# Kernel tuning notes

Measured on AMD Instinct MI355X. Metric: run time of the kernel, lower is better.

The kernel has to match this reference:

```python
import jax, jax.numpy as jnp
import numpy as np

# Module constants (from init_kwargs / defaults)
OUT_SIZE = (4, 32, 32)      # (Z, X, Y) grid
REAL_SIZE = (3.0, 25.0, 25.0)
SCALE = 1.4
THRESHOLD = 0.5
D_ELEMS = np.array([0.74 * SCALE, 0.528 * SCALE], dtype=np.float32)  # per-element match/NMS radius (O, H)


def _transform(x):
    """(B, X, Y, Z, 4*E) -> coords (B, E, N, 3), conf (B, E, N); N = Z*X*Y."""
    B, X, Y, Z, L = x.shape
    E = L // 4
    v = x.reshape(B, X, Y, Z, E, 4).transpose(0, 4, 3, 1, 2, 5)   # (B,E,Z,X,Y,4)
    v = v[..., jnp.array([2, 0, 1, 3])]                            # reorder last dim
    Zs, Xs, Ys = OUT_SIZE
    ind = jnp.stack(jnp.meshgrid(jnp.arange(Zs), jnp.arange(Xs), jnp.arange(Ys), indexing='ij'),
                    axis=-1).astype(x.dtype)                       # (Z,X,Y,3) == torch nonzero of ones
    expand = jnp.array([r / o for o, r in zip(OUT_SIZE, REAL_SIZE)], dtype=x.dtype)
    coords = (v[..., :3] + ind) * expand
    conf = v[..., 3]
    N = Zs * Xs * Ys
    return coords.reshape(B, E, N, 3), conf.reshape(B, E, N)


def _sort_by_conf(coords, conf):
    order = jnp.argsort(-conf, axis=-1)
    coords = jnp.take_along_axis(coords, order[..., None], axis=2)
    conf = jnp.take_along_axis(conf, order, axis=-1)
    return coords, conf


def _nms(pts, valid, d):
    """Greedy sequential NMS on one (N,3) point set. Point b is suppressed if any
    still-selected earlier point a<b lies within distance d. Invalid points never suppress."""
    N = pts.shape[0]
    d2 = jnp.sum((pts[:, None, :] - pts[None, :, :]) ** 2, axis=-1)   # (N,N)
    ar = jnp.arange(N)
    M = (d2 < d * d) & valid[:, None] & valid[None, :] & (ar[:, None] < ar[None, :])

    def body(b, sel):
        return sel.at[b].set(~jnp.any(sel & M[:, b]))

    sel = jax.lax.fori_loop(0, N, body, jnp.ones((N,), bool))
    return sel & valid


def _match(P, T, keepP, keepT, d):
    """Greedy row-major bipartite matching: each pred (in order) grabs the first
    still-unmatched target within distance d. Returns (TP, FP, FN) masks."""
    N = P.shape[0]
    d2 = jnp.sum((P[:, None, :] - T[None, :, :]) ** 2, axis=-1)      # (N,N)
    D = (d2 < d * d) & keepP[:, None] & keepT[None, :]

    def body(a, carry):
        selP, selT = carry
        avail = D[a] & ~selT
        has = jnp.any(avail)
        j = jnp.argmax(avail)                    # first available target index
        selT = selT.at[j].set(selT[j] | has)
        selP = selP.at[a].set(has)
        return (selP, selT)

    selP, selT = jax.lax.fori_loop(0, N, body,
                                   (jnp.zeros((N,), bool), jnp.zeros((N,), bool)))
    return selP, keepP & ~selP, keepT & ~selT    # TP, FP, FN masks


def setup_inputs() -> dict:
    key = jax.random.key(0)
    k1, k2 = jax.random.split(key)
    B = 4
    predictions = jax.random.normal(k1, (B, 32, 32, 4, 8), dtype=jnp.float32)
    targets = jax.random.normal(k2, (B, 32, 32, 4, 8), dtype=jnp.float32)
    return {"predictions": predictions, "targets": targets}


def reference(predictions, targets):
    Pc, Pconf = _sort_by_conf(*_transform(predictions))   # (B,E,N,3), (B,E,N)
    Tc, Tconf = _sort_by_conf(*_transform(targets))
    validP = Pconf > THRESHOLD
    validT = Tconf > THRESHOLD
    d = jnp.asarray(D_ELEMS)                               # (E,)

    nms_be = jax.vmap(jax.vmap(_nms, in_axes=(0, 0, 0)), in_axes=(0, 0, None))
    keepP = nms_be(Pc, validP, d)                          # (B,E,N) bool
    keepT = nms_be(Tc, validT, d)

    match_be = jax.vmap(jax.vmap(_match, in_axes=(0, 0, 0, 0, 0)), in_axes=(0, 0, 0, 0, None))
    tp, fp, fn = match_be(Pc, Tc, keepP, keepT, d)         # (B,E,N) bool each

    # sorted real-space points, NMS-kept masks, and TP/FP/FN masks (fixed-shape
    # equivalents of the torch module's filtered P/T/TP/FP/FN lists)
    return Pc, Tc, keepP, keepT, tp, fp, fn
```

## Files before the change

kernel.cpp:

```cpp
#include <hip/hip_runtime.h>
#include <hip/hip_bf16.h>

#pragma clang fp contract(off)

#define NPTS 4096
#define BE   8
#define COORD_SZ (BE * NPTS * 3)
#define MASK_SZ  (BE * NPTS)
#define OFF_PC   0
#define OFF_TC   (COORD_SZ)
#define OFF_KP   (2 * COORD_SZ)
#define OFF_KT   (2 * COORD_SZ + MASK_SZ)
#define OFF_TP   (2 * COORD_SZ + 2 * MASK_SZ)
#define OFF_FP   (2 * COORD_SZ + 3 * MASK_SZ)
#define OFF_FN   (2 * COORD_SZ + 4 * MASK_SZ)

#define VCAP 1664
#define NW   26

#define WS_KEYS_OFF  0ull
#define WS_V_OFF     524288ull
#define WS_KEEP_OFF  524352ull
#define WS_PP_OFF    528448ull
#define WS_PT_OFF    6066240ull
#define WS_NEED      8835136ull

typedef unsigned long long u64;

__device__ __forceinline__ float get_dd(int e) {
    const float d0 = (float)(0.74 * 1.4);
    const float d1 = (float)(0.528 * 1.4);
    float d = (e == 0) ? d0 : d1;
    return d * d;
}

__global__ __launch_bounds__(1024)
void sort_kernel(const float* __restrict__ pred,
                 const float* __restrict__ targ,
                 float* __restrict__ out,
                 int* __restrict__ Vcnt) {
    __shared__ u64 bufA[NPTS], bufB[NPTS];
    __shared__ unsigned int hist[1024];
    __shared__ unsigned int offarr[1024];
    __shared__ int wsum[16];
    __shared__ int vtot;
    const int s = blockIdx.x;
    const int arr = s & 1, be = s >> 1;
    const int b = be >> 1, e = be & 1;
    const float* __restrict__ src = arr ? targ : pred;
    const int t = threadIdx.x;
    const int lane = t & 63, wv = t >> 6;

    if (t == 0) vtot = 0;
    for (int n = t; n < NPTS; n += 1024) {
        int z = n >> 10, r = n & 1023, x = r >> 5, y = r & 31;
        int base = (((b * 32 + x) * 32 + y) * 4 + z) * 8 + e * 4;
        float conf = src[base + 3];
        unsigned int bits = __float_as_uint(conf);
        unsigned int u = (bits & 0x80000000u) ? ~bits : (bits | 0x80000000u);
        bufA[n] = ((u64)(~u) << 32) | (unsigned int)n;
    }
    __syncthreads();

    const u64 lmask = (1ull << lane) - 1ull;
    for (int k = 0; k < 8; ++k) {
        u64* cur = (k & 1) ? bufB : bufA;
        u64* nxt = (k & 1) ? bufA : bufB;
        const int shift = 32 + (k << 2);
        hist[t] = 0u;
        __syncthreads();

        u64 item[4]; int dg[4]; int rnk[4];
        #pragma unroll
        for (int m = 0; m < 4; ++m) {
            u64 it = cur[m * 1024 + t];
            int d = (int)((it >> shift) & 15);
            u64 eq = ~0ull;
            #pragma unroll
            for (int bb = 0; bb < 4; ++bb) {
                u64 bal = __ballot((d >> bb) & 1);
                eq &= ((d >> bb) & 1) ? bal : ~bal;
            }
            int r = (int)__popcll(eq & lmask);
            if (r == 0) hist[d * 64 + m * 16 + wv] = (unsigned int)__popcll(eq);
            item[m] = it; dg[m] = d; rnk[m] = r;
        }
        __syncthreads();

        {
            int v = (int)hist[t];
            int inc = v;
            #pragma unroll
            for (int dd = 1; dd < 64; dd <<= 1) {
                int x2 = __shfl_up(inc, dd);
                if (lane >= dd) inc += x2;
            }
            if (lane == 63) wsum[wv] = inc;
            __syncthreads();
            if (t < 16) {
                int wtot = wsum[t]; int iv = wtot;
                #pragma unroll
                for (int dd = 1; dd < 16; dd <<= 1) {
                    int x2 = __shfl_up(iv, dd);
                    if (t >= dd) iv += x2;
                }
                wsum[t] = iv - wtot;
            }
            __syncthreads();
            offarr[t] = (unsigned int)(wsum[wv] + (inc - v));
        }
        __syncthreads();

        #pragma unroll
        for (int m = 0; m < 4; ++m) {
            int pos = (int)offarr[dg[m] * 64 + m * 16 + wv] + rnk[m];
            nxt[pos] = item[m];
        }
        __syncthreads();
    }

    int myv = 0;
    for (int p = t; p < NPTS; p += 1024) {
        u64 key = bufA[p];
        int n = (int)(key & 0xFFFFFFFFull);
        myv += ((unsigned int)(key >> 32) < 0x40FFFFFFu) ? 1 : 0;
        int z = n >> 10, rr = n & 1023, x = rr >> 5, y = rr & 31;
        int base = (((b * 32 + x) * 32 + y) * 4 + z) * 8 + e * 4;
        float r0 = src[base + 0], r1 = src[base + 1], r2 = src[base + 2];
        float c0 = (r2 + (float)z) * 0.75f;
        float c1 = (r0 + (float)x) * 0.78125f;
        float c2 = (r1 + (float)y) * 0.78125f;
        float* dst = out + (size_t)arr * COORD_SZ + ((size_t)be * NPTS + p) * 3;
        dst[0] = c0; dst[1] = c1; dst[2] = c2;
    }
    atomicAdd(&vtot, myv);
    __syncthreads();
    if (t == 0) Vcnt[s] = vtot;
}

__global__ __launch_bounds__(256)
void matrix_kernel(const float* __restrict__ out,
                   const int* __restrict__ Vcnt,
                   u64* __restrict__ ws64) {
    __shared__ float4 tcol[VCAP];
    __shared__ float rowc[64][3];
    const int bx = blockIdx.x;
    const int j = bx / 26, c = bx % 26;
    const int t = threadIdx.x;

    int sRow, sCol, e;
    u64* dstBase;
    if (j < 16) {
        sRow = j; sCol = j; e = (j >> 1) & 1;
        dstBase = ws64 + (WS_PP_OFF / 8) + (size_t)j * VCAP * NW;
    } else {
        int be = j - 16;
        sRow = be * 2 + 0; sCol = be * 2 + 1; e = be & 1;
        dstBase = ws64 + (WS_PT_OFF / 8) + (size_t)be * VCAP * NW;
    }
    int Vr = Vcnt[sRow]; if (Vr > VCAP) Vr = VCAP;
    int Vc = Vcnt[sCol]; if (Vc > VCAP) Vc = VCAP;
    const int rb = c * 64;
    if (rb >= Vr) return;
    const float dd = get_dd(e);

    const float* __restrict__ colc = out + (size_t)(sCol & 1) * COORD_SZ + (size_t)(sCol >> 1) * NPTS * 3;
    const float* __restrict__ rowp = out + (size_t)(sRow & 1) * COORD_SZ + (size_t)(sRow >> 1) * NPTS * 3;

    for (int idx = t; idx < Vc * 3; idx += 256) {
        float v = colc[idx];
        int p = idx / 3, k = idx % 3;
        ((float*)&tcol[p])[k] = v;
    }
    for (int idx = t; idx < 192; idx += 256) {
        int i = idx / 3, k = idx % 3;
        if (rb + i < Vr) rowc[i][k] = rowp[(rb + i) * 3 + k];
    }
    __syncthreads();

    const int NWc = (Vc + 63) >> 6;
    const int wlimit = (j < 16) ? (c + 1) : NWc;
    const int i = t & 63;
    const bool rowOK = (rb + i) < Vr;
    if (rowOK) {
        float ax = rowc[i][0], ay = rowc[i][1], az = rowc[i][2];
        u64* dstRow = dstBase + (size_t)(rb + i) * NW;
        for (int w = t >> 6; w < wlimit; w += 4) {
            int jbase = w << 6;
            int jmax = Vc - jbase; if (jmax > 64) jmax = 64;
            u64 m = 0ull;
            for (int jj = 0; jj < jmax; ++jj) {
                float4 tc = tcol[jbase + jj];
                float dx = ax - tc.x, dy = ay - tc.y, dz = az - tc.z;
                float d2 = dx * dx + dy * dy + dz * dz;
                m |= (d2 < dd) ? (1ull << jj) : 0ull;
            }
            dstRow[w] = m;
        }
    }
}

__global__ __launch_bounds__(1024)
void nms_rounds_kernel(float* __restrict__ out,
                       const int* __restrict__ Vcnt,
                       u64* __restrict__ ws64) {
    __shared__ u64 U[NW];
    __shared__ u64 K[NW];
    __shared__ int remaining;
    const int s = blockIdx.x;
    const int arr = s & 1, be = s >> 1;
    const int t = threadIdx.x;
    int V = Vcnt[s]; if (V > VCAP) V = VCAP;
    const u64* __restrict__ Mx = ws64 + (WS_PP_OFF / 8) + (size_t)s * VCAP * NW;

    if (t < NW) {
        int base = t << 6;
        int rem = V - base;
        u64 u = (rem >= 64) ? ~0ull : ((rem > 0) ? ((1ull << rem) - 1ull) : 0ull);
        U[t] = u;
        K[t] = 0ull;
    }
    if (t == 0) remaining = V;
    __syncthreads();

    while (remaining > 0) {
        bool dec0 = false, keep0 = false;
        bool dec1 = false, keep1 = false;

        {
            const int i = t;
            if (i < V && ((U[i >> 6] >> (i & 63)) & 1ull)) {
                const u64* __restrict__ row = Mx + (size_t)i * NW;
                const int wi = i >> 6;
                u64 cu = 0ull, ck = 0ull;
                int w = 0;
                for (; w + 4 <= wi; w += 4) {
                    u64 m0 = row[w], m1 = row[w + 1], m2 = row[w + 2], m3 = row[w + 3];
                    cu |= (m0 & U[w]) | (m1 & U[w + 1]) | (m2 & U[w + 2]) | (m3 & U[w + 3]);
                    ck |= (m0 & K[w]) | (m1 & K[w + 1]) | (m2 & K[w + 2]) | (m3 & K[w + 3]);
                }
                for (; w < wi; ++w) {
                    u64 m = row[w];
                    cu |= m & U[w];
                    ck |= m & K[w];
                }
                u64 low = (1ull << (i & 63)) - 1ull;
                u64 md = row[wi] & low;
                cu |= md & U[wi];
                ck |= md & K[wi];
                if (cu == 0ull) { dec0 = true; keep0 = (ck == 0ull); }
            }
        }
        {
            const int i = t + 1024;
            if (i < V && ((U[i >> 6] >> (i & 63)) & 1ull)) {
                const u64* __restrict__ row = Mx + (size_t)i * NW;
                const int wi = i >> 6;
                u64 cu = 0ull, ck = 0ull;
                int w = 0;
                for (; w + 4 <= wi; w += 4) {
                    u64 m0 = row[w], m1 = row[w + 1], m2 = row[w + 2], m3 = row[w + 3];
                    cu |= (m0 & U[w]) | (m1 & U[w + 1]) | (m2 & U[w + 2]) | (m3 & U[w + 3]);
                    ck |= (m0 & K[w]) | (m1 & K[w + 1]) | (m2 & K[w + 2]) | (m3 & K[w + 3]);
                }
                for (; w < wi; ++w) {
                    u64 m = row[w];
                    cu |= m & U[w];
                    ck |= m & K[w];
                }
                u64 low = (1ull << (i & 63)) - 1ull;
                u64 md = row[wi] & low;
                cu |= md & U[wi];
                ck |= md & K[wi];
                if (cu == 0ull) { dec1 = true; keep1 = (ck == 0ull); }
            }
        }
        __syncthreads();

        int ndec = 0;
        if (dec0) {
            const int i = t;
            atomicAnd(&U[i >> 6], ~(1ull << (i & 63)));
            if (keep0) atomicOr(&K[i >> 6], 1ull << (i & 63));
            ndec++;
        }
        if (dec1) {
            const int i = t + 1024;
            atomicAnd(&U[i >> 6], ~(1ull << (i & 63)));
            if (keep1) atomicOr(&K[i >> 6], 1ull << (i & 63));
            ndec++;
        }
        if (ndec) atomicSub(&remaining, ndec);
        __syncthreads();
    }

    u64* kb = ws64 + (WS_KEEP_OFF / 8) + s * 32;
    if (t < 32) kb[t] = (t < NW) ? K[t] : 0ull;
    const size_t kbase = (arr == 0 ? OFF_KP : OFF_KT) + (size_t)be * NPTS;
    for (int p = t; p < NPTS; p += 1024) {
        bool k = (p < V) && ((K[p >> 6] >> (p & 63)) & 1ull);
        out[kbase + p] = k ? 1.0f : 0.0f;
    }
}

__global__ __launch_bounds__(1024)
void match_resolve_kernel(float* __restrict__ out,
                          const int* __restrict__ Vcnt,
                          u64* __restrict__ ws64) {
    __shared__ unsigned short cand[VCAP][16];
    __shared__ unsigned short candcnt[VCAP];
    __shared__ unsigned short rowlist[VCAP];
    __shared__ unsigned int colmin[VCAP];
    __shared__ u64 kPw[NW], kTw[NW], availT[NW];
    __shared__ int wp[NW];
    __shared__ int Mcnt, remaining;
    __shared__ unsigned int selP32[128];
    const int be = blockIdx.x;
    const int t = threadIdx.x;
    int Vp = Vcnt[be * 2 + 0]; if (Vp > VCAP) Vp = VCAP;
    int Vt = Vcnt[be * 2 + 1]; if (Vt > VCAP) Vt = VCAP;
    const int NWt = (Vt + 63) >> 6;
    const u64* __restrict__ PT = ws64 + (WS_PT_OFF / 8) + (size_t)be * VCAP * NW;

    if (t < NW) {
        kPw[t] = ws64[(WS_KEEP_OFF / 8) + (be * 2 + 0) * 32 + t];
        kTw[t] = ws64[(WS_KEEP_OFF / 8) + (be * 2 + 1) * 32 + t];
    }
    if (t < 128) selP32[t] = 0u;
    __syncthreads();

    if (t < 64) {
        int cP = (t < NW) ? __popcll(kPw[t]) : 0;
        int o = cP;
        for (int d = 1; d < 64; d <<= 1) {
            int v = __shfl_up(o, d);
            if (t >= d) o += v;
        }
        if (t < NW) wp[t] = o - cP;
        if (t == NW - 1) Mcnt = o;
    }
    __syncthreads();
    const int M = Mcnt;

    for (int a = t; a < Vp; a += 1024) {
        int w = a >> 6, bb = a & 63;
        u64 word = kPw[w];
        if ((word >> bb) & 1ull) {
            int pos = wp[w] + __popcll(word & ((1ull << bb) - 1ull));
            rowlist[pos] = (unsigned short)a;
        }
    }
    if (t < NW) availT[t] = kTw[t];
    if (t == 0) remaining = M;
    __syncthreads();

    #pragma unroll
    for (int half = 0; half < 2; ++half) {
        int g = t + half * 1024;
        if (g < M) {
            const u64* __restrict__ prow = PT + (size_t)rowlist[g] * NW;
            int cnt = 0;
            for (int w = 0; w < NWt; ++w) {
                u64 m = prow[w] & kTw[w];
                while (m) {
                    int bb = (int)__builtin_ctzll(m); m &= m - 1ull;
                    if (cnt < 16) cand[g][cnt] = (unsigned short)((w << 6) + bb);
                    cnt++;
                }
            }
            candcnt[g] = (unsigned short)(cnt > 16 ? 16 : cnt);
        }
    }
    __syncthreads();

    bool und0 = (t < M);
    bool und1 = (t + 1024 < M);

    while (remaining > 0) {
        for (int idx = t; idx < VCAP; idx += 1024) colmin[idx] = 0xFFFFFFFFu;
        __syncthreads();

        int jt0 = -1, jt1 = -1;
        bool dead0 = false, dead1 = false;
        if (und0) {
            const int g = t;
            int cn = candcnt[g];
            for (int k = 0; k < cn; ++k) {
                int j = cand[g][k];
                if ((availT[j >> 6] >> (j & 63)) & 1ull) {
                    if (jt0 < 0) jt0 = j;
                    atomicMin(&colmin[j], (unsigned int)g);
                }
            }
            if (jt0 < 0) dead0 = true;
        }
        if (und1) {
            const int g = t + 1024;
            int cn = candcnt[g];
            for (int k = 0; k < cn; ++k) {
                int j = cand[g][k];
                if ((availT[j >> 6] >> (j & 63)) & 1ull) {
                    if (jt1 < 0) jt1 = j;
                    atomicMin(&colmin[j], (unsigned int)g);
                }
            }
            if (jt1 < 0) dead1 = true;
        }
        __syncthreads();

        int ndec = 0;
        if (und0) {
            const int g = t;
            if (dead0) { und0 = false; ndec++; }
            else if (colmin[jt0] == (unsigned int)g) {
                atomicAnd(&availT[jt0 >> 6], ~(1ull << (jt0 & 63)));
                int a = rowlist[g];
                atomicOr(&selP32[a >> 5], 1u << (a & 31));
                und0 = false; ndec++;
            }
        }
        if (und1) {
            const int g = t + 1024;
            if (dead1) { und1 = false; ndec++; }
            else if (colmin[jt1] == (unsigned int)g) {
                atomicAnd(&availT[jt1 >> 6], ~(1ull << (jt1 & 63)));
                int a = rowlist[g];
                atomicOr(&selP32[a >> 5], 1u << (a & 31));
                und1 = false; ndec++;
            }
        }
        if (ndec) atomicSub(&remaining, ndec);
        __syncthreads();
    }

    for (int n = t; n < NPTS; n += 1024) {
        int w = n >> 6;
        bool kpb = (w < NW) && ((kPw[w] >> (n & 63)) & 1ull);
        bool tpb = (selP32[n >> 5] >> (n & 31)) & 1u;
        bool fnb = (w < NW) && ((availT[w] >> (n & 63)) & 1ull);
        size_t o = (size_t)be * NPTS + n;
        out[OFF_TP + o] = tpb ? 1.0f : 0.0f;
        out[OFF_FP + o] = (kpb && !tpb) ? 1.0f : 0.0f;
        out[OFF_FN + o] = fnb ? 1.0f : 0.0f;
    }
}

#define FVCAP 2048
#define FNWMAX (FVCAP / 64)

__global__ __launch_bounds__(1024)
void sortnms_fallback(const float* __restrict__ pred,
                      const float* __restrict__ targ,
                      float* __restrict__ out,
                      u64* __restrict__ keepbits) {
    __shared__ u64 skey[NPTS];
    __shared__ float px[FVCAP], py[FVCAP], pz[FVCAP];
    __shared__ u64 kept[FNWMAX];
    __shared__ u64 mchunk[64];
    __shared__ int supp[64];
    __shared__ int vcnt;
    const int blk = blockIdx.x;
    const int arr = blk & 1;
    const int be  = blk >> 1;
    const int b = be >> 1, e = be & 1;
    const float* __restrict__ src = arr ? targ : pred;
    const int t = threadIdx.x;
    const float dd = get_dd(e);
    if (t == 0) vcnt = 0;

    for (int n = t; n < NPTS; n += 1024) {
        int z = n >> 10, r = n & 1023, x = r >> 5, y = r & 31;
        int base = (((b * 32 + x) * 32 + y) * 4 + z) * 8 + e * 4;
        float conf = src[base + 3];
        unsigned int bits = __float_as_uint(conf);
        unsigned int u = (bits & 0x80000000u) ? ~bits : (bits | 0x80000000u);
        skey[n] = ((u64)(~u) << 32) | (unsigned int)n;
    }
    __syncthreads();
    for (int k = 2; k <= NPTS; k <<= 1) {
        for (int j = k >> 1; j > 0; j >>= 1) {
            for (int i = t; i < NPTS; i += 1024) {
                int ixj = i ^ j;
                if (ixj > i) {
                    u64 a = skey[i], c = skey[ixj];
                    bool up = ((i & k) == 0);
                    if ((a > c) == up) { skey[i] = c; skey[ixj] = a; }
                }
            }
            __syncthreads();
        }
    }
    int myv = 0;
    for (int p = t; p < NPTS; p += 1024) {
        u64 key = skey[p];
        int n = (int)(key & 0xFFFFFFFFu);
        unsigned int u = ~(unsigned int)(key >> 32);
        myv += (u > 0xBF000000u) ? 1 : 0;
        int z = n >> 10, r = n & 1023, x = r >> 5, y = r & 31;
        int base = (((b * 32 + x) * 32 + y) * 4 + z) * 8 + e * 4;
        float r0 = src[base + 0], r1 = src[base + 1], r2 = src[base + 2];
        float c0 = (r2 + (float)z) * 0.75f;
        float c1 = (r0 + (float)x) * 0.78125f;
        float c2 = (r1 + (float)y) * 0.78125f;
        float* dst = out + (size_t)arr * COORD_SZ + ((size_t)be * NPTS + p) * 3;
        dst[0] = c0; dst[1] = c1; dst[2] = c2;
        if (p < FVCAP) { px[p] = c0; py[p] = c1; pz[p] = c2; }
    }
    atomicAdd(&vcnt, myv);
    if (t < FNWMAX) kept[t] = 0ull;
    __syncthreads();

    int V = vcnt; if (V > FVCAP) V = FVCAP;
    const int nchunks = (V + 63) >> 6;
    for (int c = 0; c < nchunks; ++c) {
        if (t < 64) supp[t] = 0;
        __syncthreads();
        {
            int i = t & 63, s = t >> 6;
            int p = (c << 6) + i;
            if (p < V) {
                float x = px[p], y = py[p], z = pz[p];
                int lim = c << 6;
                bool f = false;
                for (int j = s; j < lim; j += 16) {
                    if ((kept[j >> 6] >> (j & 63)) & 1ull) {
                        float dx = x - px[j], dy = y - py[j], dz = z - pz[j];
                        float d2 = dx * dx + dy * dy + dz * dz;
                        if (d2 < dd) { f = true; break; }
                    }
                }
                if (f) atomicOr(&supp[i], 1);
            }
        }
        __syncthreads();
        if (t < 64) {
            int p = (c << 6) + t;
            u64 m = 0ull;
            if (p < V) {
                float x = px[p], y = py[p], z = pz[p];
                for (int j = 0; j < t; ++j) {
                    int q = (c << 6) + j;
                    float dx = x - px[q], dy = y - py[q], dz = z - pz[q];
                    float d2 = dx * dx + dy * dy + dz * dz;
                    if (d2 < dd) m |= (1ull << j);
                }
            }
            mchunk[t] = m;
        }
        __syncthreads();
        if (t == 0) {
            u64 kw = 0ull;
            int lim = V - (c << 6); if (lim > 64) lim = 64;
            for (int i = 0; i < lim; ++i) {
                bool ki = (supp[i] == 0) && ((mchunk[i] & kw) == 0ull);
                if (ki) kw |= (1ull << i);
            }
            kept[c] = kw;
        }
        __syncthreads();
    }
    const size_t kbase = (arr == 0 ? OFF_KP : OFF_KT) + (size_t)be * NPTS;
    for (int p = t; p < NPTS; p += 1024) {
        bool kb = (p < V) && ((kept[(p >> 6) & (FNWMAX - 1)] >> (p & 63)) & 1ull);
        out[kbase + p] = kb ? 1.0f : 0.0f;
    }
    if (t < 64) keepbits[blk * 64 + t] = (t < FNWMAX) ? kept[t] : 0ull;
}

__global__ __launch_bounds__(1024)
void match_fallback(float* __restrict__ out,
                    const u64* __restrict__ keepbits) {
    __shared__ float tx[FVCAP], ty[FVCAP], tz[FVCAP];
    __shared__ unsigned short tj[FVCAP];
    __shared__ unsigned short aidx[FVCAP];
    __shared__ unsigned short matchPos[FVCAP];
    __shared__ u64 Mask[64][FNWMAX + 1];
    __shared__ u64 kPm[64], kTm[64];
    __shared__ unsigned int selP32[128], selT32[128];
    __shared__ int wpT[64], wpP[64];
    __shared__ int Mcnt2, Kcnt2;
    __shared__ float pcx[64], pcy[64], pcz[64];
    const int be = blockIdx.x;
    const int e = be & 1;
    const int t = threadIdx.x;
    const float dd = get_dd(e);
    const float* __restrict__ Pc = out + OFF_PC + (size_t)be * NPTS * 3;
    const float* __restrict__ Tc = out + OFF_TC + (size_t)be * NPTS * 3;

    if (t < 64) {
        kPm[t] = keepbits[(be * 2 + 0) * 64 + t];
        kTm[t] = keepbits[(be * 2 + 1) * 64 + t];
    }
    if (t < 128) { selP32[t] = 0u; selT32[t] = 0u; }
    __syncthreads();
    if (t < 64) {
        int cT = __popcll(kTm[t]), cP = __popcll(kPm[t]);
        int oT = cT, oP = cP;
        for (int d = 1; d < 64; d <<= 1) {
            int vT = __shfl_up(oT, d);
            int vP = __shfl_up(oP, d);
            if (t >= d) { oT += vT; oP += vP; }
        }
        wpT[t] = oT - cT;
        wpP[t] = oP - cP;
        if (t == 63) {
            Kcnt2 = (oT > FVCAP) ? FVCAP : oT;
            Mcnt2 = (oP > FVCAP) ? FVCAP : oP;
        }
    }
    __syncthreads();
    const int K = Kcnt2, M = Mcnt2;
    for (int n = t; n < NPTS; n += 1024) {
        int w = n >> 6, bb = n & 63;
        u64 bit = 1ull << bb, lowm = bit - 1ull;
        u64 wT = kTm[w], wP = kPm[w];
        if (wT & bit) {
            int pos = wpT[w] + __popcll(wT & lowm);
            if (pos < FVCAP) {
                tx[pos] = Tc[n * 3 + 0];
                ty[pos] = Tc[n * 3 + 1];
                tz[pos] = Tc[n * 3 + 2];
                tj[pos] = (unsigned short)n;
            }
        }
        if (wP & bit) {
            int pos = wpP[w] + __popcll(wP & lowm);
            if (pos < FVCAP) aidx[pos] = (unsigned short)n;
        }
    }
    __syncthreads();

    const int NWc = (K + 63) >> 6;
    const int nchunks = (M + 63) >> 6;
    u64 selTw = 0ull;

    for (int c = 0; c < nchunks; ++c) {
        int cnt = M - (c << 6); if (cnt > 64) cnt = 64;
        if (t < 64 && t < cnt) {
            int a = aidx[(c << 6) + t];
            pcx[t] = Pc[a * 3 + 0];
            pcy[t] = Pc[a * 3 + 1];
            pcz[t] = Pc[a * 3 + 2];
        }
        __syncthreads();
        {
            int i = t & 63, s = t >> 6;
            if (i < cnt) {
                float ax = pcx[i], ay = pcy[i], az = pcz[i];
                for (int w = s; w < NWc; w += 16) {
                    int jmax = K - (w << 6); if (jmax > 64) jmax = 64;
                    int base = w << 6;
                    u64 m = 0ull;
                    for (int jj = 0; jj < jmax; ++jj) {
                        float dx = ax - tx[base + jj];
                        float dy = ay - ty[base + jj];
                        float dz = az - tz[base + jj];
                        float d2 = dx * dx + dy * dy + dz * dz;
                        m |= (d2 < dd) ? (1ull << jj) : 0ull;
                    }
                    Mask[i][w] = m;
                }
            }
        }
        __syncthreads();
        if (t < 64) {
            u64 mnext = (cnt > 0 && t < NWc) ? Mask[0][t] : 0ull;
            for (int i = 0; i < cnt; ++i) {
                u64 mrow = mnext;
                mnext = (i + 1 < cnt && t < NWc) ? Mask[i + 1][t] : 0ull;
                u64 avail = mrow & ~selTw;
                u64 bal = __ballot(avail != 0ull);
                if (bal) {
                    int w0 = (int)__builtin_ctzll(bal);
                    if (t == w0) {
                        int bb = (int)__builtin_ctzll(avail);
                        selTw |= 1ull << bb;
                        matchPos[(c << 6) + i] = (unsigned short)((w0 << 6) + bb);
                    }
                } else if (t == 0) {
                    matchPos[(c << 6) + i] = 0xffffu;
                }
            }
        }
        __syncthreads();
    }
    for (int g = t; g < M; g += 1024) {
        unsigned short pos = matchPos[g];
        if (pos != 0xffffu) {
            int jj = tj[pos];
            int a  = aidx[g];
            atomicOr(&selT32[jj >> 5], 1u << (jj & 31));
            atomicOr(&selP32[a >> 5],  1u << (a & 31));
        }
    }
    __syncthreads();
    for (int n = t; n < NPTS; n += 1024) {
        bool kpb = (kPm[n >> 6] >> (n & 63)) & 1ull;
        bool ktb = (kTm[n >> 6] >> (n & 63)) & 1ull;
        bool tpb = (selP32[n >> 5] >> (n & 31)) & 1u;
        bool stb = (selT32[n >> 5] >> (n & 31)) & 1u;
        size_t o = (size_t)be * NPTS + n;
        out[OFF_TP + o] = tpb ? 1.0f : 0.0f;
        out[OFF_FP + o] = (kpb && !tpb) ? 1.0f : 0.0f;
        out[OFF_FN + o] = (ktb && !stb) ? 1.0f : 0.0f;
    }
}

extern "C" void kernel_launch(void* const* d_in, const int* in_sizes, int n_in,
                              void* d_out, int out_size, void* d_ws, size_t ws_size,
                              hipStream_t stream) {
    const float* pred = (const float*)d_in[0];
    const float* targ = (const float*)d_in[1];
    float* out = (float*)d_out;

    if (ws_size >= WS_NEED) {
        int* Vcnt = (int*)((char*)d_ws + WS_V_OFF);
        u64* ws64 = (u64*)d_ws;

        sort_kernel<<<16, 1024, 0, stream>>>(pred, targ, out, Vcnt);
        matrix_kernel<<<624, 256, 0, stream>>>(out, Vcnt, ws64);
        nms_rounds_kernel<<<16, 1024, 0, stream>>>(out, Vcnt, ws64);
        match_resolve_kernel<<<8, 1024, 0, stream>>>(out, Vcnt, ws64);
    } else {
        u64* keepbits = (u64*)d_ws;
        sortnms_fallback<<<16, 1024, 0, stream>>>(pred, targ, out, keepbits);
        match_fallback<<<8, 1024, 0, stream>>>(out, keepbits);
    }
}
```

Measured before the change: 163.8 us.

## Replace global adjacency bitmatrices with in-shared neighbor lists for NMS and matching

Drops the separate matrix kernel that wrote dense pairwise bitmasks to global workspace. NMS now loads coordinates into shared memory and builds a capped per-point neighbor list before running its rounds. Matching computes candidate targets directly against compacted kept targets in shared memory. Round-stamped atomicMin keys remove the per-round colmin reset and its barrier. This cuts a kernel launch and global traffic, but the O(V^2) distance work now runs on only 16 or 8 blocks instead of 624, so the compute is far less parallel.

```diff
diff --git a/kernel.cpp b/kernel.cpp
--- a/kernel.cpp
+++ b/kernel.cpp
@@ -18,12 +18,11 @@
 #define VCAP 1664
 #define NW   26
 
-#define WS_KEYS_OFF  0ull
 #define WS_V_OFF     524288ull
 #define WS_KEEP_OFF  524352ull
-#define WS_PP_OFF    528448ull
-#define WS_PT_OFF    6066240ull
-#define WS_NEED      8835136ull
+#define WS_NEED      528448ull
+
+#define NBCAP 24
 
 typedef unsigned long long u64;
 
@@ -138,141 +137,82 @@
     if (t == 0) Vcnt[s] = vtot;
 }
 
-__global__ __launch_bounds__(256)
-void matrix_kernel(const float* __restrict__ out,
-                   const int* __restrict__ Vcnt,
-                   u64* __restrict__ ws64) {
-    __shared__ float4 tcol[VCAP];
-    __shared__ float rowc[64][3];
-    const int bx = blockIdx.x;
-    const int j = bx / 26, c = bx % 26;
-    const int t = threadIdx.x;
-
-    int sRow, sCol, e;
-    u64* dstBase;
-    if (j < 16) {
-        sRow = j; sCol = j; e = (j >> 1) & 1;
-        dstBase = ws64 + (WS_PP_OFF / 8) + (size_t)j * VCAP * NW;
-    } else {
-        int be = j - 16;
-        sRow = be * 2 + 0; sCol = be * 2 + 1; e = be & 1;
-        dstBase = ws64 + (WS_PT_OFF / 8) + (size_t)be * VCAP * NW;
-    }
-    int Vr = Vcnt[sRow]; if (Vr > VCAP) Vr = VCAP;
-    int Vc = Vcnt[sCol]; if (Vc > VCAP) Vc = VCAP;
-    const int rb = c * 64;
-    if (rb >= Vr) return;
-    const float dd = get_dd(e);
-
-    const float* __restrict__ colc = out + (size_t)(sCol & 1) * COORD_SZ + (size_t)(sCol >> 1) * NPTS * 3;
-    const float* __restrict__ rowp = out + (size_t)(sRow & 1) * COORD_SZ + (size_t)(sRow >> 1) * NPTS * 3;
-
-    for (int idx = t; idx < Vc * 3; idx += 256) {
-        float v = colc[idx];
-        int p = idx / 3, k = idx % 3;
-        ((float*)&tcol[p])[k] = v;
-    }
-    for (int idx = t; idx < 192; idx += 256) {
-        int i = idx / 3, k = idx % 3;
-        if (rb + i < Vr) rowc[i][k] = rowp[(rb + i) * 3 + k];
-    }
-    __syncthreads();
-
-    const int NWc = (Vc + 63) >> 6;
-    const int wlimit = (j < 16) ? (c + 1) : NWc;
-    const int i = t & 63;
-    const bool rowOK = (rb + i) < Vr;
-    if (rowOK) {
-        float ax = rowc[i][0], ay = rowc[i][1], az = rowc[i][2];
-        u64* dstRow = dstBase + (size_t)(rb + i) * NW;
-        for (int w = t >> 6; w < wlimit; w += 4) {
-            int jbase = w << 6;
-            int jmax = Vc - jbase; if (jmax > 64) jmax = 64;
-            u64 m = 0ull;
-            for (int jj = 0; jj < jmax; ++jj) {
-                float4 tc = tcol[jbase + jj];
-                float dx = ax - tc.x, dy = ay - tc.y, dz = az - tc.z;
-                float d2 = dx * dx + dy * dy + dz * dz;
-                m |= (d2 < dd) ? (1ull << jj) : 0ull;
-            }
-            dstRow[w] = m;
-        }
-    }
-}
-
 __global__ __launch_bounds__(1024)
-void nms_rounds_kernel(float* __restrict__ out,
-                       const int* __restrict__ Vcnt,
-                       u64* __restrict__ ws64) {
-    __shared__ u64 U[NW];
-    __shared__ u64 K[NW];
+void nms_kernel(float* __restrict__ out,
+                const int* __restrict__ Vcnt,
+                u64* __restrict__ ws64) {
+    __shared__ float px[VCAP], py[VCAP], pz[VCAP];
+    __shared__ unsigned short nbr[VCAP][NBCAP];
+    __shared__ unsigned short nbrcnt[VCAP];
+    __shared__ u64 U[NW], K[NW];
     __shared__ int remaining;
     const int s = blockIdx.x;
     const int arr = s & 1, be = s >> 1;
     const int t = threadIdx.x;
     int V = Vcnt[s]; if (V > VCAP) V = VCAP;
-    const u64* __restrict__ Mx = ws64 + (WS_PP_OFF / 8) + (size_t)s * VCAP * NW;
-
+    const float dd = get_dd(be & 1);
+
+    const float* __restrict__ src = out + (size_t)arr * COORD_SZ + (size_t)be * NPTS * 3;
+    for (int idx = t; idx < V * 3; idx += 1024) {
+        float v = src[idx];
+        int p = idx / 3, k = idx - p * 3;
+        if (k == 0) px[p] = v; else if (k == 1) py[p] = v; else pz[p] = v;
+    }
     if (t < NW) {
-        int base = t << 6;
-        int rem = V - base;
-        u64 u = (rem >= 64) ? ~0ull : ((rem > 0) ? ((1ull << rem) - 1ull) : 0ull);
-        U[t] = u;
+        int rem = V - (t << 6);
+        U[t] = (rem >= 64) ? ~0ull : ((rem > 0) ? ((1ull << rem) - 1ull) : 0ull);
         K[t] = 0ull;
     }
     if (t == 0) remaining = V;
     __syncthreads();
 
+    #pragma unroll
+    for (int half = 0; half < 2; ++half) {
+        int i = t + half * 1024;
+        if (i < V) {
+            float ax = px[i], ay = py[i], az = pz[i];
+            int cnt = 0;
+            for (int j = 0; j < i; ++j) {
+                float dx = ax - px[j], dy = ay - py[j], dz = az - pz[j];
+                float d2 = dx * dx + dy * dy + dz * dz;
+                if (d2 < dd) { if (cnt < NBCAP) nbr[i][cnt] = (unsigned short)j; cnt++; }
+            }
+            nbrcnt[i] = (unsigned short)cnt;
+        }
+    }
+    __syncthreads();
+
     while (remaining > 0) {
-        bool dec0 = false, keep0 = false;
-        bool dec1 = false, keep1 = false;
-
-        {
-            const int i = t;
+        bool dec0 = false, keep0 = false, dec1 = false, keep1 = false;
+        #pragma unroll
+        for (int half = 0; half < 2; ++half) {
+            const int i = t + half * 1024;
             if (i < V && ((U[i >> 6] >> (i & 63)) & 1ull)) {
-                const u64* __restrict__ row = Mx + (size_t)i * NW;
-                const int wi = i >> 6;
-                u64 cu = 0ull, ck = 0ull;
-                int w = 0;
-                for (; w + 4 <= wi; w += 4) {
-                    u64 m0 = row[w], m1 = row[w + 1], m2 = row[w + 2], m3 = row[w + 3];
-                    cu |= (m0 & U[w]) | (m1 & U[w + 1]) | (m2 & U[w + 2]) | (m3 & U[w + 3]);
-                    ck |= (m0 & K[w]) | (m1 & K[w + 1]) | (m2 & K[w + 2]) | (m3 & K[w + 3]);
-                }
-                for (; w < wi; ++w) {
-                    u64 m = row[w];
-                    cu |= m & U[w];
-                    ck |= m & K[w];
-                }
-                u64 low = (1ull << (i & 63)) - 1ull;
-                u64 md = row[wi] & low;
-                cu |= md & U[wi];
-                ck |= md & K[wi];
-                if (cu == 0ull) { dec0 = true; keep0 = (ck == 0ull); }
-            }
-        }
-        {
-            const int i = t + 1024;
-            if (i < V && ((U[i >> 6] >> (i & 63)) & 1ull)) {
-                const u64* __restrict__ row = Mx + (size_t)i * NW;
-                const int wi = i >> 6;
-                u64 cu = 0ull, ck = 0ull;
-                int w = 0;
-                for (; w + 4 <= wi; w += 4) {
-                    u64 m0 = row[w], m1 = row[w + 1], m2 = row[w + 2], m3 = row[w + 3];
-                    cu |= (m0 & U[w]) | (m1 & U[w + 1]) | (m2 & U[w + 2]) | (m3 & U[w + 3]);
-                    ck |= (m0 & K[w]) | (m1 & K[w + 1]) | (m2 & K[w + 2]) | (m3 & K[w + 3]);
-                }
-                for (; w < wi; ++w) {
-                    u64 m = row[w];
-                    cu |= m & U[w];
-                    ck |= m & K[w];
-                }
-                u64 low = (1ull << (i & 63)) - 1ull;
-                u64 md = row[wi] & low;
-                cu |= md & U[wi];
-                ck |= md & K[wi];
-                if (cu == 0ull) { dec1 = true; keep1 = (ck == 0ull); }
+                bool cu = false, ck = false;
+                int cnt = nbrcnt[i];
+                if (cnt <= NBCAP) {
+                    for (int k = 0; k < cnt; ++k) {
+                        int j = nbr[i][k];
+                        u64 bit = 1ull << (j & 63);
+                        cu = cu || ((U[j >> 6] & bit) != 0ull);
+                        ck = ck || ((K[j >> 6] & bit) != 0ull);
+                    }
+                } else {
+                    float ax = px[i], ay = py[i], az = pz[i];
+                    for (int j = 0; j < i; ++j) {
+                        float dx = ax - px[j], dy = ay - py[j], dz = az - pz[j];
+                        float d2 = dx * dx + dy * dy + dz * dz;
+                        if (d2 < dd) {
+                            u64 bit = 1ull << (j & 63);
+                            cu = cu || ((U[j >> 6] & bit) != 0ull);
+                            ck = ck || ((K[j >> 6] & bit) != 0ull);
+                        }
+                    }
+                }
+                if (!cu) {
+                    if (half == 0) { dec0 = true; keep0 = !ck; }
+                    else           { dec1 = true; keep1 = !ck; }
+                }
             }
         }
         __syncthreads();
@@ -307,66 +247,81 @@
 void match_resolve_kernel(float* __restrict__ out,
                           const int* __restrict__ Vcnt,
                           u64* __restrict__ ws64) {
+    __shared__ float tx[VCAP], ty[VCAP], tz[VCAP];
+    __shared__ unsigned short tposs[VCAP];
     __shared__ unsigned short cand[VCAP][16];
     __shared__ unsigned short candcnt[VCAP];
     __shared__ unsigned short rowlist[VCAP];
     __shared__ unsigned int colmin[VCAP];
     __shared__ u64 kPw[NW], kTw[NW], availT[NW];
-    __shared__ int wp[NW];
-    __shared__ int Mcnt, remaining;
+    __shared__ int wpP[NW], wpT[NW];
+    __shared__ int Mcnt, Kcnt, remaining;
     __shared__ unsigned int selP32[128];
     const int be = blockIdx.x;
     const int t = threadIdx.x;
     int Vp = Vcnt[be * 2 + 0]; if (Vp > VCAP) Vp = VCAP;
     int Vt = Vcnt[be * 2 + 1]; if (Vt > VCAP) Vt = VCAP;
-    const int NWt = (Vt + 63) >> 6;
-    const u64* __restrict__ PT = ws64 + (WS_PT_OFF / 8) + (size_t)be * VCAP * NW;
+    const float dd = get_dd(be & 1);
 
     if (t < NW) {
         kPw[t] = ws64[(WS_KEEP_OFF / 8) + (be * 2 + 0) * 32 + t];
         kTw[t] = ws64[(WS_KEEP_OFF / 8) + (be * 2 + 1) * 32 + t];
     }
     if (t < 128) selP32[t] = 0u;
+    for (int idx = t; idx < VCAP; idx += 1024) colmin[idx] = 0xFFFFFFFFu;
     __syncthreads();
 
     if (t < 64) {
         int cP = (t < NW) ? __popcll(kPw[t]) : 0;
-        int o = cP;
+        int cT = (t < NW) ? __popcll(kTw[t]) : 0;
+        int oP = cP, oT = cT;
         for (int d = 1; d < 64; d <<= 1) {
-            int v = __shfl_up(o, d);
-            if (t >= d) o += v;
-        }
-        if (t < NW) wp[t] = o - cP;
-        if (t == NW - 1) Mcnt = o;
-    }
-    __syncthreads();
-    const int M = Mcnt;
+            int vP = __shfl_up(oP, d);
+            int vT = __shfl_up(oT, d);
+            if (t >= d) { oP += vP; oT += vT; }
+        }
+        if (t < NW) { wpP[t] = oP - cP; wpT[t] = oT - cT; }
+        if (t == NW - 1) { Mcnt = oP; Kcnt = oT; }
+    }
+    __syncthreads();
+    const int M = Mcnt, Kt = Kcnt;
 
     for (int a = t; a < Vp; a += 1024) {
         int w = a >> 6, bb = a & 63;
         u64 word = kPw[w];
         if ((word >> bb) & 1ull) {
-            int pos = wp[w] + __popcll(word & ((1ull << bb) - 1ull));
+            int pos = wpP[w] + __popcll(word & ((1ull << bb) - 1ull));
             rowlist[pos] = (unsigned short)a;
         }
     }
+    const float* __restrict__ Tc = out + OFF_TC + (size_t)be * NPTS * 3;
+    for (int n = t; n < Vt; n += 1024) {
+        int w = n >> 6, bb = n & 63;
+        u64 word = kTw[w];
+        if ((word >> bb) & 1ull) {
+            int pos = wpT[w] + __popcll(word & ((1ull << bb) - 1ull));
+            tx[pos] = Tc[n * 3 + 0];
+            ty[pos] = Tc[n * 3 + 1];
+            tz[pos] = Tc[n * 3 + 2];
+            tposs[pos] = (unsigned short)n;
+        }
+    }
     if (t < NW) availT[t] = kTw[t];
-    if (t == 0) remaining = M;
-    __syncthreads();
-
+    if (t == 0) remaining = Mcnt;
+    __syncthreads();
+
+    const float* __restrict__ Pc = out + OFF_PC + (size_t)be * NPTS * 3;
     #pragma unroll
     for (int half = 0; half < 2; ++half) {
         int g = t + half * 1024;
         if (g < M) {
-            const u64* __restrict__ prow = PT + (size_t)rowlist[g] * NW;
+            int a = rowlist[g];
+            float ax = Pc[a * 3 + 0], ay = Pc[a * 3 + 1], az = Pc[a * 3 + 2];
             int cnt = 0;
-            for (int w = 0; w < NWt; ++w) {
-                u64 m = prow[w] & kTw[w];
-                while (m) {
-                    int bb = (int)__builtin_ctzll(m); m &= m - 1ull;
-                    if (cnt < 16) cand[g][cnt] = (unsigned short)((w << 6) + bb);
-                    cnt++;
-                }
+            for (int k = 0; k < Kt; ++k) {
+                float dx = ax - tx[k], dy = ay - ty[k], dz = az - tz[k];
+                float d2 = dx * dx + dy * dy + dz * dz;
+                if (d2 < dd) { if (cnt < 16) cand[g][cnt] = tposs[k]; cnt++; }
             }
             candcnt[g] = (unsigned short)(cnt > 16 ? 16 : cnt);
         }
@@ -375,11 +330,10 @@
 
     bool und0 = (t < M);
     bool und1 = (t + 1024 < M);
+    int round = 0;
 
     while (remaining > 0) {
-        for (int idx = t; idx < VCAP; idx += 1024) colmin[idx] = 0xFFFFFFFFu;
-        __syncthreads();
-
+        const unsigned int stampBase = (unsigned int)(4095 - round) << 11;
         int jt0 = -1, jt1 = -1;
         bool dead0 = false, dead1 = false;
         if (und0) {
@@ -389,7 +343,7 @@
                 int j = cand[g][k];
                 if ((availT[j >> 6] >> (j & 63)) & 1ull) {
                     if (jt0 < 0) jt0 = j;
-                    atomicMin(&colmin[j], (unsigned int)g);
+                    atomicMin(&colmin[j], stampBase | (unsigned int)g);
                 }
             }
             if (jt0 < 0) dead0 = true;
@@ -401,7 +355,7 @@
                 int j = cand[g][k];
                 if ((availT[j >> 6] >> (j & 63)) & 1ull) {
                     if (jt1 < 0) jt1 = j;
-                    atomicMin(&colmin[j], (unsigned int)g);
+                    atomicMin(&colmin[j], stampBase | (unsigned int)g);
                 }
             }
             if (jt1 < 0) dead1 = true;
@@ -412,7 +366,7 @@
         if (und0) {
             const int g = t;
             if (dead0) { und0 = false; ndec++; }
-            else if (colmin[jt0] == (unsigned int)g) {
+            else if (colmin[jt0] == (stampBase | (unsigned int)g)) {
                 atomicAnd(&availT[jt0 >> 6], ~(1ull << (jt0 & 63)));
                 int a = rowlist[g];
                 atomicOr(&selP32[a >> 5], 1u << (a & 31));
@@ -422,7 +376,7 @@
         if (und1) {
             const int g = t + 1024;
             if (dead1) { und1 = false; ndec++; }
-            else if (colmin[jt1] == (unsigned int)g) {
+            else if (colmin[jt1] == (stampBase | (unsigned int)g)) {
                 atomicAnd(&availT[jt1 >> 6], ~(1ull << (jt1 & 63)));
                 int a = rowlist[g];
                 atomicOr(&selP32[a >> 5], 1u << (a & 31));
@@ -430,6 +384,7 @@
             }
         }
         if (ndec) atomicSub(&remaining, ndec);
+        ++round;
         __syncthreads();
     }
 
@@ -718,8 +673,7 @@
         u64* ws64 = (u64*)d_ws;
 
         sort_kernel<<<16, 1024, 0, stream>>>(pred, targ, out, Vcnt);
-        matrix_kernel<<<624, 256, 0, stream>>>(out, Vcnt, ws64);
-        nms_rounds_kernel<<<16, 1024, 0, stream>>>(out, Vcnt, ws64);
+        nms_kernel<<<16, 1024, 0, stream>>>(out, Vcnt, ws64);
         match_resolve_kernel<<<8, 1024, 0, stream>>>(out, Vcnt, ws64);
     } else {
         u64* keepbits = (u64*)d_ws;
```

Result: slower. 351.9 us (+114.8%).

## Use shared-memory neighbor lists for NMS rounds and round-stamped colmin in matching

Applied to the files above, without the earlier changes.

NMS now builds a per-point list of earlier neighbors (up to 16) in shared memory once, then each round checks only those neighbors' U/K bits instead of rescanning the global bitmask row. Points with no neighbors are kept immediately before the loop, and rows with more than 16 neighbors fall back to the bitmask scan. In matching, colmin is initialized once and entries carry a decreasing round stamp, which removes the per-round reset and one barrier. The neighbor table costs about 56KB of shared memory, and the stamp scheme assumes fewer than 4096 rounds.

```diff
diff --git a/kernel.cpp b/kernel.cpp
--- a/kernel.cpp
+++ b/kernel.cpp
@@ -18,12 +18,13 @@
 #define VCAP 1664
 #define NW   26
 
-#define WS_KEYS_OFF  0ull
 #define WS_V_OFF     524288ull
 #define WS_KEEP_OFF  524352ull
 #define WS_PP_OFF    528448ull
 #define WS_PT_OFF    6066240ull
 #define WS_NEED      8835136ull
+
+#define NBC 16
 
 typedef unsigned long long u64;
 
@@ -204,6 +205,8 @@
 void nms_rounds_kernel(float* __restrict__ out,
                        const int* __restrict__ Vcnt,
                        u64* __restrict__ ws64) {
+    __shared__ unsigned short nbr[VCAP][NBC];
+    __shared__ unsigned short nbrcnt[VCAP];
     __shared__ u64 U[NW];
     __shared__ u64 K[NW];
     __shared__ int remaining;
@@ -214,80 +217,99 @@
     const u64* __restrict__ Mx = ws64 + (WS_PP_OFF / 8) + (size_t)s * VCAP * NW;
 
     if (t < NW) {
-        int base = t << 6;
-        int rem = V - base;
-        u64 u = (rem >= 64) ? ~0ull : ((rem > 0) ? ((1ull << rem) - 1ull) : 0ull);
-        U[t] = u;
+        int rem = V - (t << 6);
+        U[t] = (rem >= 64) ? ~0ull : ((rem > 0) ? ((1ull << rem) - 1ull) : 0ull);
         K[t] = 0ull;
     }
     if (t == 0) remaining = V;
     __syncthreads();
 
-    while (remaining > 0) {
-        bool dec0 = false, keep0 = false;
-        bool dec1 = false, keep1 = false;
-
-        {
-            const int i = t;
-            if (i < V && ((U[i >> 6] >> (i & 63)) & 1ull)) {
-                const u64* __restrict__ row = Mx + (size_t)i * NW;
-                const int wi = i >> 6;
-                u64 cu = 0ull, ck = 0ull;
-                int w = 0;
-                for (; w + 4 <= wi; w += 4) {
-                    u64 m0 = row[w], m1 = row[w + 1], m2 = row[w + 2], m3 = row[w + 3];
-                    cu |= (m0 & U[w]) | (m1 & U[w + 1]) | (m2 & U[w + 2]) | (m3 & U[w + 3]);
-                    ck |= (m0 & K[w]) | (m1 & K[w + 1]) | (m2 & K[w + 2]) | (m3 & K[w + 3]);
-                }
-                for (; w < wi; ++w) {
-                    u64 m = row[w];
-                    cu |= m & U[w];
-                    ck |= m & K[w];
-                }
-                u64 low = (1ull << (i & 63)) - 1ull;
-                u64 md = row[wi] & low;
-                cu |= md & U[wi];
-                ck |= md & K[wi];
-                if (cu == 0ull) { dec0 = true; keep0 = (ck == 0ull); }
-            }
-        }
-        {
-            const int i = t + 1024;
-            if (i < V && ((U[i >> 6] >> (i & 63)) & 1ull)) {
-                const u64* __restrict__ row = Mx + (size_t)i * NW;
-                const int wi = i >> 6;
-                u64 cu = 0ull, ck = 0ull;
-                int w = 0;
-                for (; w + 4 <= wi; w += 4) {
-                    u64 m0 = row[w], m1 = row[w + 1], m2 = row[w + 2], m3 = row[w + 3];
-                    cu |= (m0 & U[w]) | (m1 & U[w + 1]) | (m2 & U[w + 2]) | (m3 & U[w + 3]);
-                    ck |= (m0 & K[w]) | (m1 & K[w + 1]) | (m2 & K[w + 2]) | (m3 & K[w + 3]);
-                }
-                for (; w < wi; ++w) {
-                    u64 m = row[w];
-                    cu |= m & U[w];
-                    ck |= m & K[w];
-                }
-                u64 low = (1ull << (i & 63)) - 1ull;
-                u64 md = row[wi] & low;
-                cu |= md & U[wi];
-                ck |= md & K[wi];
-                if (cu == 0ull) { dec1 = true; keep1 = (ck == 0ull); }
-            }
-        }
-        __syncthreads();
-
+    bool dec0 = false, dec1 = false;
+    #pragma unroll
+    for (int half = 0; half < 2; ++half) {
+        const int i = t + half * 1024;
+        if (i < V) {
+            const u64* __restrict__ row = Mx + (size_t)i * NW;
+            const int wi = i >> 6;
+            int cnt = 0;
+            for (int w = 0; w <= wi; ++w) {
+                u64 m = row[w];
+                if (w == wi) m &= (1ull << (i & 63)) - 1ull;
+                while (m) {
+                    int bb = (int)__builtin_ctzll(m); m &= m - 1ull;
+                    if (cnt < NBC) nbr[i][cnt] = (unsigned short)((w << 6) + bb);
+                    cnt++;
+                }
+            }
+            nbrcnt[i] = (unsigned short)cnt;
+            if (cnt == 0) { if (half == 0) dec0 = true; else dec1 = true; }
+        }
+    }
+    __syncthreads();
+    {
         int ndec = 0;
         if (dec0) {
             const int i = t;
             atomicAnd(&U[i >> 6], ~(1ull << (i & 63)));
-            if (keep0) atomicOr(&K[i >> 6], 1ull << (i & 63));
+            atomicOr(&K[i >> 6], 1ull << (i & 63));
             ndec++;
         }
         if (dec1) {
             const int i = t + 1024;
             atomicAnd(&U[i >> 6], ~(1ull << (i & 63)));
-            if (keep1) atomicOr(&K[i >> 6], 1ull << (i & 63));
+            atomicOr(&K[i >> 6], 1ull << (i & 63));
+            ndec++;
+        }
+        if (ndec) atomicSub(&remaining, ndec);
+    }
+    __syncthreads();
+
+    while (remaining > 0) {
+        bool d0 = false, k0 = false, d1 = false, k1 = false;
+        #pragma unroll
+        for (int half = 0; half < 2; ++half) {
+            const int i = t + half * 1024;
+            if (i < V && ((U[i >> 6] >> (i & 63)) & 1ull)) {
+                bool cu = false, ck = false;
+                int cnt = nbrcnt[i];
+                if (cnt <= NBC) {
+                    for (int k = 0; k < cnt; ++k) {
+                        int j = nbr[i][k];
+                        u64 bit = 1ull << (j & 63);
+                        cu = cu || ((U[j >> 6] & bit) != 0ull);
+                        ck = ck || ((K[j >> 6] & bit) != 0ull);
+                    }
+                } else {
+                    const u64* __restrict__ row = Mx + (size_t)i * NW;
+                    const int wi = i >> 6;
+                    u64 cuw = 0ull, ckw = 0ull;
+                    for (int w = 0; w <= wi; ++w) {
+                        u64 m = row[w];
+                        if (w == wi) m &= (1ull << (i & 63)) - 1ull;
+                        cuw |= m & U[w];
+                        ckw |= m & K[w];
+                    }
+                    cu = cuw != 0ull; ck = ckw != 0ull;
+                }
+                if (!cu) {
+                    if (half == 0) { d0 = true; k0 = !ck; }
+                    else           { d1 = true; k1 = !ck; }
+                }
+            }
+        }
+        __syncthreads();
+
+        int ndec = 0;
+        if (d0) {
+            const int i = t;
+            atomicAnd(&U[i >> 6], ~(1ull << (i & 63)));
+            if (k0) atomicOr(&K[i >> 6], 1ull << (i & 63));
+            ndec++;
+        }
+        if (d1) {
+            const int i = t + 1024;
+            atomicAnd(&U[i >> 6], ~(1ull << (i & 63)));
+            if (k1) atomicOr(&K[i >> 6], 1ull << (i & 63));
             ndec++;
         }
         if (ndec) atomicSub(&remaining, ndec);
@@ -327,6 +349,7 @@
         kTw[t] = ws64[(WS_KEEP_OFF / 8) + (be * 2 + 1) * 32 + t];
     }
     if (t < 128) selP32[t] = 0u;
+    for (int idx = t; idx < VCAP; idx += 1024) colmin[idx] = 0xFFFFFFFFu;
     __syncthreads();
 
     if (t < 64) {
@@ -375,11 +398,10 @@
 
     bool und0 = (t < M);
     bool und1 = (t + 1024 < M);
+    int round = 0;
 
     while (remaining > 0) {
-        for (int idx = t; idx < VCAP; idx += 1024) colmin[idx] = 0xFFFFFFFFu;
-        __syncthreads();
-
+        const unsigned int stampBase = (unsigned int)(4095 - round) << 11;
         int jt0 = -1, jt1 = -1;
         bool dead0 = false, dead1 = false;
         if (und0) {
@@ -389,7 +411,7 @@
                 int j = cand[g][k];
                 if ((availT[j >> 6] >> (j & 63)) & 1ull) {
                     if (jt0 < 0) jt0 = j;
-                    atomicMin(&colmin[j], (unsigned int)g);
+                    atomicMin(&colmin[j], stampBase | (unsigned int)g);
                 }
             }
             if (jt0 < 0) dead0 = true;
@@ -401,7 +423,7 @@
                 int j = cand[g][k];
                 if ((availT[j >> 6] >> (j & 63)) & 1ull) {
                     if (jt1 < 0) jt1 = j;
-                    atomicMin(&colmin[j], (unsigned int)g);
+                    atomicMin(&colmin[j], stampBase | (unsigned int)g);
                 }
             }
             if (jt1 < 0) dead1 = true;
@@ -412,7 +434,7 @@
         if (und0) {
             const int g = t;
             if (dead0) { und0 = false; ndec++; }
-            else if (colmin[jt0] == (unsigned int)g) {
+            else if (colmin[jt0] == (stampBase | (unsigned int)g)) {
                 atomicAnd(&availT[jt0 >> 6], ~(1ull << (jt0 & 63)));
                 int a = rowlist[g];
                 atomicOr(&selP32[a >> 5], 1u << (a & 31));
@@ -422,7 +444,7 @@
         if (und1) {
             const int g = t + 1024;
             if (dead1) { und1 = false; ndec++; }
-            else if (colmin[jt1] == (unsigned int)g) {
+            else if (colmin[jt1] == (stampBase | (unsigned int)g)) {
                 atomicAnd(&availT[jt1 >> 6], ~(1ull << (jt1 & 63)));
                 int a = rowlist[g];
                 atomicOr(&selP32[a >> 5], 1u << (a & 31));
@@ -430,6 +452,7 @@
             }
         }
         if (ndec) atomicSub(&remaining, ndec);
+        ++round;
         __syncthreads();
     }
 
```

Result: slower. 171.4 us (+4.6%).
